# Optimization experiments

Measured on AMD Instinct MI355X. Metric: run time of the kernel, lower is better.

## Reference

```python
import jax, jax.numpy as jnp
import numpy as np

N = 524288   # tokens (accounts)
D = 9        # num_prop_size
E = 2        # expert_size
H = 128      # expert MLP hidden
M = 32       # moe_out
O = 2        # output_size
K = 1        # top-k
LOSS_COF = 0.01
EPS = 1e-10


def setup_inputs() -> dict:
    key = jax.random.key(0)
    ks = jax.random.split(key, 10)
    f32 = jnp.float32
    return {
        "num_prop": jax.random.normal(ks[0], (N, D), f32),
        "cat_prop": jax.random.normal(ks[1], (N, 3), f32),
        "w_gate": jax.random.normal(ks[2], (D, E), f32) * 0.1,
        "W1": jax.random.normal(ks[3], (E, D, H), f32) * 0.1,
        "b1": jax.random.normal(ks[4], (E, H), f32) * 0.01,
        "W2": jax.random.normal(ks[5], (E, H, M), f32) * 0.1,
        "b2": jax.random.normal(ks[6], (E, M), f32) * 0.01,
        "Wout": jax.random.normal(ks[7], (M, O), f32) * 0.1,
        "bout": jax.random.normal(ks[8], (O,), f32) * 0.01,
        "k": K,
    }


def _cv_squared(x):
    # torch: x.var() (unbiased) / (x.mean()**2 + eps)
    return jnp.var(x, ddof=1) / (jnp.mean(x) ** 2 + EPS)


def reference(num_prop, cat_prop, w_gate, W1, b1, W2, b2, Wout, bout, k):
    x = num_prop                                   # eval mode: dropout = identity
    n, e = x.shape[0], w_gate.shape[1]

    # --- top-k gating (eval: clean logits, no noise) ---
    logits = x @ w_gate                            # [N, E]
    top_logits, top_idx = jax.lax.top_k(logits, min(k + 1, e))
    top_k_gates = jax.nn.softmax(top_logits[:, :k], axis=1)   # [N, k]
    rows = jnp.arange(n)[:, None]
    gates = jnp.zeros_like(logits).at[rows, top_idx[:, :k]].set(top_k_gates)  # [N, E]

    importance = gates.sum(axis=0)                 # [E]
    load = (gates > 0).astype(jnp.float32).sum(axis=0)  # [E]
    loss = (_cv_squared(importance) + _cv_squared(load)) * LOSS_COF

    # --- experts: per-expert 2-layer MLP, computed dense (E=2) then gated combine ---
    h = jax.nn.relu(jnp.einsum("nd,edh->neh", x, W1) + b1)    # [N, E, H]
    y_e = jnp.einsum("neh,ehm->nem", h, W2) + b2              # [N, E, M]
    y = jnp.einsum("ne,nem->nm", gates, y_e)                  # [N, M]

    out = y @ Wout + bout                                     # [N, O]
    return (out, loss)
```

## Files before the change

kernel.cpp:

```cpp
#include <hip/hip_runtime.h>

#define NTOK 524288
#define TPB  256
#define NBLK (NTOK / TPB)

__device__ __forceinline__ float bf2f(unsigned short u) {
    union { unsigned int i; float f; } v;
    v.i = ((unsigned int)u) << 16;
    return v.f;
}

__device__ __forceinline__ float ldq(const void* p, int i, bool f32) {
    if (f32) return ((const float*)p)[i];
    return bf2f(((const unsigned short*)p)[i]);
}

__global__ void prep_kernel(const void* __restrict__ num_prop,
                            const void* __restrict__ wgate,
                            const void* __restrict__ W1,
                            const void* __restrict__ b1,
                            const void* __restrict__ W2,
                            const void* __restrict__ b2,
                            const void* __restrict__ Wout,
                            const void* __restrict__ bout,
                            unsigned int* __restrict__ cnt1,
                            int* __restrict__ flag,
                            float* __restrict__ bpp,
                            float* __restrict__ wgf,
                            float* __restrict__ wpack)
{
    __shared__ unsigned int bad;
    __shared__ int sflag;
    const int t = threadIdx.x;
    if (t == 0) { bad = 0u; *cnt1 = 0u; }
    __syncthreads();
    if (t < 72) {
        const unsigned short* u = (const unsigned short*)num_prop;
        int e = (u[t] >> 7) & 0xFF;
        if (e < 64 || e > 191) atomicOr(&bad, 1u);
    }
    __syncthreads();
    if (t == 0) { sflag = (int)bad; *flag = (int)bad; }
    __syncthreads();
    const bool f32 = (sflag != 0);

    if (t < 18) wgf[t] = ldq(wgate, t, f32);

    if (t < 4) {
        int e = t >> 1, o = t & 1;
        float acc = ldq(bout, o, f32);
        for (int m = 0; m < 32; ++m)
            acc += ldq(b2, e * 32 + m, f32) * ldq(Wout, m * 2 + o, f32);
        bpp[t] = acc;
    }

    const int e = t >> 7;
    const int j = t & 127;
    float p0 = 0.f, p1 = 0.f;
    for (int m = 0; m < 32; ++m) {
        float w = ldq(W2, (e * 128 + j) * 32 + m, f32);
        p0 += w * ldq(Wout, m * 2 + 0, f32);
        p1 += w * ldq(Wout, m * 2 + 1, f32);
    }
    float* dst = wpack + e * 1536 + j * 12;
    #pragma unroll
    for (int d = 0; d < 9; ++d)
        dst[d] = ldq(W1, (e * 9 + d) * 128 + j, f32);
    dst[9]  = ldq(b1, e * 128 + j, f32);
    dst[10] = p0;
    dst[11] = p1;
}

__global__ __launch_bounds__(TPB, 8)
void moe_main(const void* __restrict__ xg,
              const int* __restrict__ flag,
              const float* __restrict__ wgf,
              const float* __restrict__ bpp,
              const float* __restrict__ wpack,
              unsigned int* __restrict__ cnt1,
              float2* __restrict__ out)
{
    __shared__ __align__(16) float xs[TPB * 9];
    __shared__ unsigned char smap[TPB];
    __shared__ unsigned int wcnt[4];

    const int tid  = threadIdx.x;
    const int lane = tid & 63;
    const int wave = tid >> 6;

    const bool f32 = (*flag) != 0;
    const int gbase = blockIdx.x * (TPB * 9);
    if (f32) {
        const float* xf = (const float*)xg;
        #pragma unroll
        for (int i = 0; i < 9; ++i)
            xs[tid + i * TPB] = xf[gbase + tid + i * TPB];
    } else {
        const unsigned short* xu = (const unsigned short*)xg;
        for (int i = tid; i < TPB * 9; i += TPB)
            xs[i] = bf2f(xu[gbase + i]);
    }
    __syncthreads();

    float l0 = 0.f, l1 = 0.f;
    #pragma unroll
    for (int d = 0; d < 9; ++d) {
        float xv = xs[tid * 9 + d];
        l0 = fmaf(xv, wgf[d * 2 + 0], l0);
        l1 = fmaf(xv, wgf[d * 2 + 1], l1);
    }
    const bool e1 = l1 > l0;

    unsigned long long bal = __ballot(e1);
    if (lane == 0) wcnt[wave] = (unsigned int)__popcll(bal);
    __syncthreads();
    int pre = 0, tot = 0;
    #pragma unroll
    for (int w = 0; w < 4; ++w) {
        int c = (int)wcnt[w];
        if (w < wave) pre += c;
        tot += c;
    }
    const int n1 = tot;
    const int n0 = TPB - n1;
    const int p1 = pre + (int)__popcll(bal & ((1ull << lane) - 1ull));
    const int slot = e1 ? (n0 + p1) : (tid - p1);
    smap[slot] = (unsigned char)tid;
    if (tid == 0) atomicAdd(cnt1, (unsigned int)n1);
    __syncthreads();

    const int t = (int)smap[tid];
    float x[9];
    #pragma unroll
    for (int d = 0; d < 9; ++d) x[d] = xs[t * 9 + d];

    const int wbase = __builtin_amdgcn_readfirstlane(tid) & 192;
    const int n0u   = __builtin_amdgcn_readfirstlane(n0);

    float2 res;
    if (n0u <= wbase || n0u >= wbase + 64) {
        const int ew = (n0u <= wbase) ? 1 : 0;
        const float* wp = wpack + ew * 1536;
        float a0 = bpp[ew * 2 + 0], a1 = bpp[ew * 2 + 1];
        #pragma unroll 2
        for (int jp = 0; jp < 64; ++jp) {
            const float* r0 = wp + jp * 24;
            const float* r1 = r0 + 12;
            float h0 = r0[9], h1 = r1[9];
            #pragma unroll
            for (int d = 0; d < 9; ++d) {
                h0 = fmaf(x[d], r0[d], h0);
                h1 = fmaf(x[d], r1[d], h1);
            }
            h0 = fmaxf(h0, 0.f);
            h1 = fmaxf(h1, 0.f);
            a0 = fmaf(h0, r0[10], a0); a1 = fmaf(h0, r0[11], a1);
            a0 = fmaf(h1, r1[10], a0); a1 = fmaf(h1, r1[11], a1);
        }
        res.x = a0; res.y = a1;
    } else {
        const bool em = (tid >= n0u);
        float a00 = bpp[0], a01 = bpp[1], a10 = bpp[2], a11 = bpp[3];
        #pragma unroll 4
        for (int j = 0; j < 128; ++j) {
            const float* r0 = wpack + j * 12;
            const float* r1 = wpack + 1536 + j * 12;
            float h0 = r0[9], h1 = r1[9];
            #pragma unroll
            for (int d = 0; d < 9; ++d) {
                h0 = fmaf(x[d], r0[d], h0);
                h1 = fmaf(x[d], r1[d], h1);
            }
            h0 = fmaxf(h0, 0.f);
            h1 = fmaxf(h1, 0.f);
            a00 = fmaf(h0, r0[10], a00); a01 = fmaf(h0, r0[11], a01);
            a10 = fmaf(h1, r1[10], a10); a11 = fmaf(h1, r1[11], a11);
        }
        res.x = em ? a10 : a00;
        res.y = em ? a11 : a01;
    }

    __syncthreads();
    ((float2*)xs)[t] = res;
    __syncthreads();
    out[blockIdx.x * TPB + tid] = ((float2*)xs)[tid];
}

__global__ void finalize_kernel(const unsigned int* __restrict__ cnt1,
                                float* __restrict__ loss_out)
{
    double c1 = (double)(*cnt1);
    double c0 = (double)NTOK - c1;
    double diff = c0 - c1;
    double mean = (double)NTOK * 0.5;
    double var  = 0.5 * diff * diff;
    double cv2  = var / (mean * mean + 1e-10);
    *loss_out = (float)(0.02 * cv2);
}

extern "C" void kernel_launch(void* const* d_in, const int* in_sizes, int n_in,
                              void* d_out, int out_size, void* d_ws, size_t ws_size,
                              hipStream_t stream) {
    const void* num_prop = d_in[0];
    const void* w_gate   = d_in[2];
    const void* W1       = d_in[3];
    const void* b1       = d_in[4];
    const void* W2       = d_in[5];
    const void* b2       = d_in[6];
    const void* Wout     = d_in[7];
    const void* bout     = d_in[8];

    char* ws = (char*)d_ws;
    unsigned int* cnt1 = (unsigned int*)ws;
    int* flag          = (int*)(ws + 8);
    float* bpp         = (float*)(ws + 16);
    float* wgf         = (float*)(ws + 64);
    float* wpack       = (float*)(ws + 192);

    float*  outf = (float*)d_out;
    float2* out2 = (float2*)d_out;

    hipLaunchKernelGGL(prep_kernel, dim3(1), dim3(256), 0, stream,
                       num_prop, w_gate, W1, b1, W2, b2, Wout, bout,
                       cnt1, flag, bpp, wgf, wpack);
    hipLaunchKernelGGL(moe_main, dim3(NBLK), dim3(TPB), 0, stream,
                       num_prop, flag, wgf, bpp, wpack, cnt1, out2);
    hipLaunchKernelGGL(finalize_kernel, dim3(1), dim3(1), 0, stream,
                       cnt1, outf + (size_t)NTOK * 2);
}
```

Baseline: 149.6 us.

## Process four tokens per thread to amortize weight loads across tokens

Each block now handles 1024 tokens with 256 threads, so every thread computes four expert-sorted tokens and each weight row load is reused across four tokens. The packed weight rows are padded to 16 floats so they can be fetched with aligned vector loads, and launch bounds drop to 2 blocks per CU to allow more registers. In exchange, mixed-expert waves are more likely because each wave now spans 256 sorted slots, and those waves run the costlier both-experts path. There are also 4x fewer blocks and higher register pressure.

```diff
diff --git a/kernel.cpp b/kernel.cpp
--- a/kernel.cpp
+++ b/kernel.cpp
@@ -2,7 +2,8 @@
 
 #define NTOK 524288
 #define TPB  256
-#define NBLK (NTOK / TPB)
+#define TOKB 1024
+#define NBLK (NTOK / TOKB)
 
 __device__ __forceinline__ float bf2f(unsigned short u) {
     union { unsigned int i; float f; } v;
@@ -62,16 +63,17 @@
         p0 += w * ldq(Wout, m * 2 + 0, f32);
         p1 += w * ldq(Wout, m * 2 + 1, f32);
     }
-    float* dst = wpack + e * 1536 + j * 12;
+    float* dst = wpack + e * 2048 + j * 16;
     #pragma unroll
     for (int d = 0; d < 9; ++d)
         dst[d] = ldq(W1, (e * 9 + d) * 128 + j, f32);
     dst[9]  = ldq(b1, e * 128 + j, f32);
     dst[10] = p0;
     dst[11] = p1;
-}
-
-__global__ __launch_bounds__(TPB, 8)
+    dst[12] = 0.f; dst[13] = 0.f; dst[14] = 0.f; dst[15] = 0.f;
+}
+
+__global__ __launch_bounds__(TPB, 2)
 void moe_main(const void* __restrict__ xg,
               const int* __restrict__ flag,
               const float* __restrict__ wgf,
@@ -80,110 +82,154 @@
               unsigned int* __restrict__ cnt1,
               float2* __restrict__ out)
 {
-    __shared__ __align__(16) float xs[TPB * 9];
-    __shared__ unsigned char smap[TPB];
-    __shared__ unsigned int wcnt[4];
+    __shared__ __align__(16) float xs[TOKB * 9];
+    __shared__ unsigned short smap[TOKB];
+    __shared__ unsigned int wcnt[16];
 
     const int tid  = threadIdx.x;
     const int lane = tid & 63;
     const int wave = tid >> 6;
 
     const bool f32 = (*flag) != 0;
-    const int gbase = blockIdx.x * (TPB * 9);
+    const int gbase = blockIdx.x * (TOKB * 9);
     if (f32) {
         const float* xf = (const float*)xg;
         #pragma unroll
-        for (int i = 0; i < 9; ++i)
+        for (int i = 0; i < 36; ++i)
             xs[tid + i * TPB] = xf[gbase + tid + i * TPB];
     } else {
         const unsigned short* xu = (const unsigned short*)xg;
-        for (int i = tid; i < TPB * 9; i += TPB)
+        for (int i = tid; i < TOKB * 9; i += TPB)
             xs[i] = bf2f(xu[gbase + i]);
     }
     __syncthreads();
 
-    float l0 = 0.f, l1 = 0.f;
+    bool e1g[4];
+    unsigned long long balg[4];
+    #pragma unroll
+    for (int g = 0; g < 4; ++g) {
+        float l0 = 0.f, l1 = 0.f;
+        #pragma unroll
+        for (int d = 0; d < 9; ++d) {
+            float xv = xs[(g * 256 + tid) * 9 + d];
+            l0 = fmaf(xv, wgf[d * 2 + 0], l0);
+            l1 = fmaf(xv, wgf[d * 2 + 1], l1);
+        }
+        e1g[g] = l1 > l0;
+        balg[g] = __ballot(e1g[g]);
+        if (lane == 0) wcnt[g * 4 + wave] = (unsigned int)__popcll(balg[g]);
+    }
+    __syncthreads();
+
+    int pres[16]; int run = 0;
+    #pragma unroll
+    for (int c = 0; c < 16; ++c) { pres[c] = run; run += (int)wcnt[c]; }
+    const int n1 = run;
+    const int n0 = TOKB - n1;
+    const unsigned long long below = (1ull << lane) - 1ull;
+    #pragma unroll
+    for (int g = 0; g < 4; ++g) {
+        const int tok = g * 256 + tid;
+        const int pr  = pres[g * 4 + wave] + (int)__popcll(balg[g] & below);
+        const int slot = e1g[g] ? (n0 + pr) : (tok - pr);
+        smap[slot] = (unsigned short)tok;
+    }
+    if (tid == 0) atomicAdd(cnt1, (unsigned int)n1);
+    __syncthreads();
+
+    const int s0 = tid * 4;
+    const int tk0 = (int)smap[s0 + 0], tk1 = (int)smap[s0 + 1];
+    const int tk2 = (int)smap[s0 + 2], tk3 = (int)smap[s0 + 3];
+    float x0[9], x1[9], x2[9], x3[9];
     #pragma unroll
     for (int d = 0; d < 9; ++d) {
-        float xv = xs[tid * 9 + d];
-        l0 = fmaf(xv, wgf[d * 2 + 0], l0);
-        l1 = fmaf(xv, wgf[d * 2 + 1], l1);
-    }
-    const bool e1 = l1 > l0;
-
-    unsigned long long bal = __ballot(e1);
-    if (lane == 0) wcnt[wave] = (unsigned int)__popcll(bal);
-    __syncthreads();
-    int pre = 0, tot = 0;
-    #pragma unroll
-    for (int w = 0; w < 4; ++w) {
-        int c = (int)wcnt[w];
-        if (w < wave) pre += c;
-        tot += c;
-    }
-    const int n1 = tot;
-    const int n0 = TPB - n1;
-    const int p1 = pre + (int)__popcll(bal & ((1ull << lane) - 1ull));
-    const int slot = e1 ? (n0 + p1) : (tid - p1);
-    smap[slot] = (unsigned char)tid;
-    if (tid == 0) atomicAdd(cnt1, (unsigned int)n1);
-    __syncthreads();
-
-    const int t = (int)smap[tid];
-    float x[9];
-    #pragma unroll
-    for (int d = 0; d < 9; ++d) x[d] = xs[t * 9 + d];
-
-    const int wbase = __builtin_amdgcn_readfirstlane(tid) & 192;
+        x0[d] = xs[tk0 * 9 + d];
+        x1[d] = xs[tk1 * 9 + d];
+        x2[d] = xs[tk2 * 9 + d];
+        x3[d] = xs[tk3 * 9 + d];
+    }
+
+    const int wslot = __builtin_amdgcn_readfirstlane(wave) << 8;
     const int n0u   = __builtin_amdgcn_readfirstlane(n0);
 
-    float2 res;
-    if (n0u <= wbase || n0u >= wbase + 64) {
-        const int ew = (n0u <= wbase) ? 1 : 0;
-        const float* wp = wpack + ew * 1536;
-        float a0 = bpp[ew * 2 + 0], a1 = bpp[ew * 2 + 1];
+    float2 r0v, r1v, r2v, r3v;
+    if (n0u <= wslot || n0u >= wslot + 256) {
+        const int ew = (n0u <= wslot) ? 1 : 0;
+        const float* wp = wpack + ew * 2048;
+        const float b0 = bpp[ew * 2 + 0], b1v = bpp[ew * 2 + 1];
+        float a00 = b0, a01 = b1v, a10 = b0, a11 = b1v;
+        float a20 = b0, a21 = b1v, a30 = b0, a31 = b1v;
         #pragma unroll 2
-        for (int jp = 0; jp < 64; ++jp) {
-            const float* r0 = wp + jp * 24;
-            const float* r1 = r0 + 12;
-            float h0 = r0[9], h1 = r1[9];
+        for (int j = 0; j < 128; ++j) {
+            const float* r = wp + j * 16;
+            float h0 = r[9], h1 = r[9], h2 = r[9], h3 = r[9];
             #pragma unroll
             for (int d = 0; d < 9; ++d) {
-                h0 = fmaf(x[d], r0[d], h0);
-                h1 = fmaf(x[d], r1[d], h1);
+                const float w = r[d];
+                h0 = fmaf(x0[d], w, h0);
+                h1 = fmaf(x1[d], w, h1);
+                h2 = fmaf(x2[d], w, h2);
+                h3 = fmaf(x3[d], w, h3);
             }
-            h0 = fmaxf(h0, 0.f);
-            h1 = fmaxf(h1, 0.f);
-            a0 = fmaf(h0, r0[10], a0); a1 = fmaf(h0, r0[11], a1);
-            a0 = fmaf(h1, r1[10], a0); a1 = fmaf(h1, r1[11], a1);
+            h0 = fmaxf(h0, 0.f); h1 = fmaxf(h1, 0.f);
+            h2 = fmaxf(h2, 0.f); h3 = fmaxf(h3, 0.f);
+            const float wa = r[10], wb = r[11];
+            a00 = fmaf(h0, wa, a00); a01 = fmaf(h0, wb, a01);
+            a10 = fmaf(h1, wa, a10); a11 = fmaf(h1, wb, a11);
+            a20 = fmaf(h2, wa, a20); a21 = fmaf(h2, wb, a21);
+            a30 = fmaf(h3, wa, a30); a31 = fmaf(h3, wb, a31);
         }
-        res.x = a0; res.y = a1;
+        r0v.x = a00; r0v.y = a01; r1v.x = a10; r1v.y = a11;
+        r2v.x = a20; r2v.y = a21; r3v.x = a30; r3v.y = a31;
     } else {
-        const bool em = (tid >= n0u);
-        float a00 = bpp[0], a01 = bpp[1], a10 = bpp[2], a11 = bpp[3];
-        #pragma unroll 4
+        float A0[4], A1[4], A2[4], A3[4];
+        #pragma unroll
+        for (int k = 0; k < 4; ++k) { A0[k] = bpp[0]; A1[k] = bpp[1]; A2[k] = bpp[2]; A3[k] = bpp[3]; }
         for (int j = 0; j < 128; ++j) {
-            const float* r0 = wpack + j * 12;
-            const float* r1 = wpack + 1536 + j * 12;
-            float h0 = r0[9], h1 = r1[9];
+            const float* p0 = wpack + j * 16;
+            const float* p1 = wpack + 2048 + j * 16;
+            float h00 = p0[9], h01 = p1[9];
+            float h10 = p0[9], h11 = p1[9];
+            float h20 = p0[9], h21 = p1[9];
+            float h30 = p0[9], h31 = p1[9];
             #pragma unroll
             for (int d = 0; d < 9; ++d) {
-                h0 = fmaf(x[d], r0[d], h0);
-                h1 = fmaf(x[d], r1[d], h1);
+                const float w0 = p0[d], w1 = p1[d];
+                h00 = fmaf(x0[d], w0, h00); h01 = fmaf(x0[d], w1, h01);
+                h10 = fmaf(x1[d], w0, h10); h11 = fmaf(x1[d], w1, h11);
+                h20 = fmaf(x2[d], w0, h20); h21 = fmaf(x2[d], w1, h21);
+                h30 = fmaf(x3[d], w0, h30); h31 = fmaf(x3[d], w1, h31);
             }
-            h0 = fmaxf(h0, 0.f);
-            h1 = fmaxf(h1, 0.f);
-            a00 = fmaf(h0, r0[10], a00); a01 = fmaf(h0, r0[11], a01);
-            a10 = fmaf(h1, r1[10], a10); a11 = fmaf(h1, r1[11], a11);
+            h00 = fmaxf(h00, 0.f); h01 = fmaxf(h01, 0.f);
+            h10 = fmaxf(h10, 0.f); h11 = fmaxf(h11, 0.f);
+            h20 = fmaxf(h20, 0.f); h21 = fmaxf(h21, 0.f);
+            h30 = fmaxf(h30, 0.f); h31 = fmaxf(h31, 0.f);
+            const float wa0 = p0[10], wb0 = p0[11], wa1 = p1[10], wb1 = p1[11];
+            A0[0] = fmaf(h00, wa0, A0[0]); A1[0] = fmaf(h00, wb0, A1[0]);
+            A2[0] = fmaf(h01, wa1, A2[0]); A3[0] = fmaf(h01, wb1, A3[0]);
+            A0[1] = fmaf(h10, wa0, A0[1]); A1[1] = fmaf(h10, wb0, A1[1]);
+            A2[1] = fmaf(h11, wa1, A2[1]); A3[1] = fmaf(h11, wb1, A3[1]);
+            A0[2] = fmaf(h20, wa0, A0[2]); A1[2] = fmaf(h20, wb0, A1[2]);
+            A2[2] = fmaf(h21, wa1, A2[2]); A3[2] = fmaf(h21, wb1, A3[2]);
+            A0[3] = fmaf(h30, wa0, A0[3]); A1[3] = fmaf(h30, wb0, A1[3]);
+            A2[3] = fmaf(h31, wa1, A2[3]); A3[3] = fmaf(h31, wb1, A3[3]);
         }
-        res.x = em ? a10 : a00;
-        res.y = em ? a11 : a01;
-    }
-
-    __syncthreads();
-    ((float2*)xs)[t] = res;
-    __syncthreads();
-    out[blockIdx.x * TPB + tid] = ((float2*)xs)[tid];
+        const bool e0s = (s0 + 0) >= n0u, e1s = (s0 + 1) >= n0u;
+        const bool e2s = (s0 + 2) >= n0u, e3s = (s0 + 3) >= n0u;
+        r0v.x = e0s ? A2[0] : A0[0]; r0v.y = e0s ? A3[0] : A1[0];
+        r1v.x = e1s ? A2[1] : A0[1]; r1v.y = e1s ? A3[1] : A1[1];
+        r2v.x = e2s ? A2[2] : A0[2]; r2v.y = e2s ? A3[2] : A1[2];
+        r3v.x = e3s ? A2[3] : A0[3]; r3v.y = e3s ? A3[3] : A1[3];
+    }
+
+    __syncthreads();
+    float2* ob = (float2*)xs;
+    ob[tk0] = r0v; ob[tk1] = r1v; ob[tk2] = r2v; ob[tk3] = r3v;
+    __syncthreads();
+    const int obase = blockIdx.x * TOKB;
+    #pragma unroll
+    for (int g = 0; g < 4; ++g)
+        out[obase + g * 256 + tid] = ob[g * 256 + tid];
 }
 
 __global__ void finalize_kernel(const unsigned int* __restrict__ cnt1,
```

Result: slower. 153.4 us (+2.6%).

## Compute expert first layer with bf16x3-split MFMA instead of scalar FMAs

Applied to the files above, without the earlier changes.

Replaces the per-thread scalar FMA hidden-layer loop with MFMA 16x16x32 bf16 instructions. Inputs and W1 are split into hi/lo bf16 parts (hi*hi + lo*hi + hi*lo), and the bias is folded in through a constant-one column, so accuracy stays close to fp32. Both experts are computed for all tokens and the gated result is selected per token, which removes the token sort and the per-wave expert branching. It also vectorises the input load with float4 and moves the load count to per-wave atomics. The cost is extra prep packing, more registers from dropping the occupancy hint, and some residual precision loss from the split-bf16 scheme.

```diff
diff --git a/kernel.cpp b/kernel.cpp
--- a/kernel.cpp
+++ b/kernel.cpp
@@ -3,16 +3,26 @@
 #define NTOK 524288
 #define TPB  256
 #define NBLK (NTOK / TPB)
+
+typedef __attribute__((ext_vector_type(8))) short short8v;
+typedef __attribute__((ext_vector_type(4))) float float4v;
+
+union FragU { uint4 u; short8v s; };
 
 __device__ __forceinline__ float bf2f(unsigned short u) {
     union { unsigned int i; float f; } v;
     v.i = ((unsigned int)u) << 16;
     return v.f;
 }
-
 __device__ __forceinline__ float ldq(const void* p, int i, bool f32) {
     if (f32) return ((const float*)p)[i];
     return bf2f(((const unsigned short*)p)[i]);
+}
+__device__ __forceinline__ unsigned short btrunc(float w) {
+    return (unsigned short)(__float_as_uint(w) >> 16);
+}
+__device__ __forceinline__ float hif(float w) {
+    return __uint_as_float(__float_as_uint(w) & 0xFFFF0000u);
 }
 
 __global__ void prep_kernel(const void* __restrict__ num_prop,
@@ -25,9 +35,11 @@
                             const void* __restrict__ bout,
                             unsigned int* __restrict__ cnt1,
                             int* __restrict__ flag,
-                            float* __restrict__ bpp,
+                            float* __restrict__ bppf,
                             float* __restrict__ wgf,
-                            float* __restrict__ wpack)
+                            float* __restrict__ w2f,
+                            float* __restrict__ wpackF,
+                            unsigned int* __restrict__ wfragB)
 {
     __shared__ unsigned int bad;
     __shared__ int sflag;
@@ -51,52 +63,101 @@
         float acc = ldq(bout, o, f32);
         for (int m = 0; m < 32; ++m)
             acc += ldq(b2, e * 32 + m, f32) * ldq(Wout, m * 2 + o, f32);
-        bpp[t] = acc;
-    }
-
-    const int e = t >> 7;
-    const int j = t & 127;
-    float p0 = 0.f, p1 = 0.f;
-    for (int m = 0; m < 32; ++m) {
-        float w = ldq(W2, (e * 128 + j) * 32 + m, f32);
-        p0 += w * ldq(Wout, m * 2 + 0, f32);
-        p1 += w * ldq(Wout, m * 2 + 1, f32);
-    }
-    float* dst = wpack + e * 1536 + j * 12;
-    #pragma unroll
-    for (int d = 0; d < 9; ++d)
-        dst[d] = ldq(W1, (e * 9 + d) * 128 + j, f32);
-    dst[9]  = ldq(b1, e * 128 + j, f32);
-    dst[10] = p0;
-    dst[11] = p1;
-}
-
-__global__ __launch_bounds__(TPB, 8)
+        bppf[t] = acc;
+    }
+
+    {
+        const int e = t >> 7, j = t & 127;
+        float p0 = 0.f, p1 = 0.f;
+        for (int m = 0; m < 32; ++m) {
+            float w = ldq(W2, (e * 128 + j) * 32 + m, f32);
+            p0 += w * ldq(Wout, m * 2 + 0, f32);
+            p1 += w * ldq(Wout, m * 2 + 1, f32);
+        }
+        w2f[e * 256 + j * 2 + 0] = p0;
+        w2f[e * 256 + j * 2 + 1] = p1;
+        float* dst = wpackF + e * 1536 + j * 12;
+        #pragma unroll
+        for (int d = 0; d < 9; ++d)
+            dst[d] = ldq(W1, (e * 9 + d) * 128 + j, f32);
+        dst[9]  = ldq(b1, e * 128 + j, f32);
+        dst[10] = p0;
+        dst[11] = p1;
+    }
+
+    for (int q = 0; q < 4; ++q) {
+        const int idx = t + q * 256;
+        const int e  = idx >> 9;
+        const int t8 = (idx >> 6) & 7;
+        const int l  = idx & 63;
+        const int j  = t8 * 16 + (l & 15);
+        const int kg = l >> 4;
+        const float bb = ldq(b1, e * 128 + j, f32);
+        unsigned int u4[4];
+        #pragma unroll
+        for (int i = 0; i < 4; ++i) {
+            unsigned short v[2];
+            #pragma unroll
+            for (int h = 0; h < 2; ++h) {
+                const int s = kg * 8 + 2 * i + h;
+                unsigned short r = 0;
+                if (s <= 8) {
+                    float w = ldq(W1, (e * 9 + s) * 128 + j, f32);
+                    r = btrunc(w);
+                } else if (s <= 17) {
+                    float w = ldq(W1, (e * 9 + (s - 9)) * 128 + j, f32);
+                    r = btrunc(w);
+                } else if (s <= 26) {
+                    float w = ldq(W1, (e * 9 + (s - 18)) * 128 + j, f32);
+                    r = btrunc(w - hif(w));
+                } else if (s == 27) {
+                    r = btrunc(bb);
+                } else if (s == 28) {
+                    r = btrunc(bb - hif(bb));
+                }
+                v[h] = r;
+            }
+            u4[i] = (unsigned int)v[0] | ((unsigned int)v[1] << 16);
+        }
+        #pragma unroll
+        for (int i = 0; i < 4; ++i) wfragB[idx * 4 + i] = u4[i];
+    }
+}
+
+__global__ __launch_bounds__(TPB)
 void moe_main(const void* __restrict__ xg,
               const int* __restrict__ flag,
               const float* __restrict__ wgf,
-              const float* __restrict__ bpp,
-              const float* __restrict__ wpack,
+              const float* __restrict__ bppf,
+              const float* __restrict__ w2f,
+              const float* __restrict__ wpackF,
+              const unsigned int* __restrict__ wfragB,
               unsigned int* __restrict__ cnt1,
               float2* __restrict__ out)
 {
     __shared__ __align__(16) float xs[TPB * 9];
-    __shared__ unsigned char smap[TPB];
-    __shared__ unsigned int wcnt[4];
+    __shared__ __align__(16) unsigned int xpk[TPB * 20];
+    __shared__ float2 ob[TPB];
+    __shared__ unsigned char eflag[TPB];
 
     const int tid  = threadIdx.x;
     const int lane = tid & 63;
     const int wave = tid >> 6;
-
     const bool f32 = (*flag) != 0;
-    const int gbase = blockIdx.x * (TPB * 9);
+    const int tbase = blockIdx.x * TPB;
+
     if (f32) {
-        const float* xf = (const float*)xg;
-        #pragma unroll
-        for (int i = 0; i < 9; ++i)
-            xs[tid + i * TPB] = xf[gbase + tid + i * TPB];
+        const float4* xf4 = (const float4*)xg;
+        float4* xsv = (float4*)xs;
+        const int g4 = blockIdx.x * (TPB * 9 / 4);
+        #pragma unroll
+        for (int i = 0; i < 3; ++i) {
+            const int idx = i * 256 + tid;
+            if (idx < TPB * 9 / 4) xsv[idx] = xf4[g4 + idx];
+        }
     } else {
         const unsigned short* xu = (const unsigned short*)xg;
+        const int gbase = blockIdx.x * (TPB * 9);
         for (int i = tid; i < TPB * 9; i += TPB)
             xs[i] = bf2f(xu[gbase + i]);
     }
@@ -105,85 +166,137 @@
     float l0 = 0.f, l1 = 0.f;
     #pragma unroll
     for (int d = 0; d < 9; ++d) {
-        float xv = xs[tid * 9 + d];
+        const float xv = xs[tid * 9 + d];
         l0 = fmaf(xv, wgf[d * 2 + 0], l0);
         l1 = fmaf(xv, wgf[d * 2 + 1], l1);
     }
     const bool e1 = l1 > l0;
-
+    eflag[tid] = e1 ? 1 : 0;
     unsigned long long bal = __ballot(e1);
-    if (lane == 0) wcnt[wave] = (unsigned int)__popcll(bal);
-    __syncthreads();
-    int pre = 0, tot = 0;
-    #pragma unroll
-    for (int w = 0; w < 4; ++w) {
-        int c = (int)wcnt[w];
-        if (w < wave) pre += c;
-        tot += c;
-    }
-    const int n1 = tot;
-    const int n0 = TPB - n1;
-    const int p1 = pre + (int)__popcll(bal & ((1ull << lane) - 1ull));
-    const int slot = e1 ? (n0 + p1) : (tid - p1);
-    smap[slot] = (unsigned char)tid;
-    if (tid == 0) atomicAdd(cnt1, (unsigned int)n1);
-    __syncthreads();
-
-    const int t = (int)smap[tid];
-    float x[9];
-    #pragma unroll
-    for (int d = 0; d < 9; ++d) x[d] = xs[t * 9 + d];
-
-    const int wbase = __builtin_amdgcn_readfirstlane(tid) & 192;
-    const int n0u   = __builtin_amdgcn_readfirstlane(n0);
-
-    float2 res;
-    if (n0u <= wbase || n0u >= wbase + 64) {
-        const int ew = (n0u <= wbase) ? 1 : 0;
-        const float* wp = wpack + ew * 1536;
-        float a0 = bpp[ew * 2 + 0], a1 = bpp[ew * 2 + 1];
-        #pragma unroll 2
-        for (int jp = 0; jp < 64; ++jp) {
-            const float* r0 = wp + jp * 24;
-            const float* r1 = r0 + 12;
+    if (lane == 0) atomicAdd(cnt1, (unsigned int)__popcll(bal));
+
+    if (!f32) {
+        float xr[9];
+        #pragma unroll
+        for (int d = 0; d < 9; ++d) xr[d] = xs[tid * 9 + d];
+        float a00 = bppf[0], a01 = bppf[1], a10 = bppf[2], a11 = bppf[3];
+        for (int j = 0; j < 128; ++j) {
+            const float* r0 = wpackF + j * 12;
+            const float* r1 = wpackF + 1536 + j * 12;
             float h0 = r0[9], h1 = r1[9];
             #pragma unroll
             for (int d = 0; d < 9; ++d) {
-                h0 = fmaf(x[d], r0[d], h0);
-                h1 = fmaf(x[d], r1[d], h1);
-            }
-            h0 = fmaxf(h0, 0.f);
-            h1 = fmaxf(h1, 0.f);
-            a0 = fmaf(h0, r0[10], a0); a1 = fmaf(h0, r0[11], a1);
-            a0 = fmaf(h1, r1[10], a0); a1 = fmaf(h1, r1[11], a1);
-        }
-        res.x = a0; res.y = a1;
-    } else {
-        const bool em = (tid >= n0u);
-        float a00 = bpp[0], a01 = bpp[1], a10 = bpp[2], a11 = bpp[3];
-        #pragma unroll 4
-        for (int j = 0; j < 128; ++j) {
-            const float* r0 = wpack + j * 12;
-            const float* r1 = wpack + 1536 + j * 12;
-            float h0 = r0[9], h1 = r1[9];
-            #pragma unroll
-            for (int d = 0; d < 9; ++d) {
-                h0 = fmaf(x[d], r0[d], h0);
-                h1 = fmaf(x[d], r1[d], h1);
-            }
-            h0 = fmaxf(h0, 0.f);
-            h1 = fmaxf(h1, 0.f);
+                h0 = fmaf(xr[d], r0[d], h0);
+                h1 = fmaf(xr[d], r1[d], h1);
+            }
+            h0 = fmaxf(h0, 0.f); h1 = fmaxf(h1, 0.f);
             a00 = fmaf(h0, r0[10], a00); a01 = fmaf(h0, r0[11], a01);
             a10 = fmaf(h1, r1[10], a10); a11 = fmaf(h1, r1[11], a11);
         }
-        res.x = em ? a10 : a00;
-        res.y = em ? a11 : a01;
-    }
-
-    __syncthreads();
-    ((float2*)xs)[t] = res;
-    __syncthreads();
-    out[blockIdx.x * TPB + tid] = ((float2*)xs)[tid];
+        out[tbase + tid] = make_float2(e1 ? a10 : a00, e1 ? a11 : a01);
+        return;
+    }
+
+    {
+        unsigned short hv[9], lv[9];
+        #pragma unroll
+        for (int d = 0; d < 9; ++d) {
+            const float xv = xs[tid * 9 + d];
+            hv[d] = btrunc(xv);
+            lv[d] = btrunc(xv - hif(xv));
+        }
+        const unsigned int ONE = 0x3F80u;
+        #define PK(a,b) ((unsigned int)(a) | ((unsigned int)(b) << 16))
+        uint4* xp = (uint4*)&xpk[tid * 20];
+        xp[0] = make_uint4(PK(hv[0],hv[1]), PK(hv[2],hv[3]),
+                           PK(hv[4],hv[5]), PK(hv[6],hv[7]));
+        xp[1] = make_uint4(PK(hv[8],lv[0]), PK(lv[1],lv[2]),
+                           PK(lv[3],lv[4]), PK(lv[5],lv[6]));
+        xp[2] = make_uint4(PK(lv[7],lv[8]), PK(hv[0],hv[1]),
+                           PK(hv[2],hv[3]), PK(hv[4],hv[5]));
+        xp[3] = make_uint4(PK(hv[6],hv[7]), PK(hv[8],ONE),
+                           PK(ONE,0u), 0u);
+        #undef PK
+    }
+    __syncthreads();
+
+    FragU bw[16];
+    #pragma unroll
+    for (int et = 0; et < 16; ++et)
+        bw[et].u = ((const uint4*)wfragB)[et * 64 + lane];
+    float2 w2v[16];
+    #pragma unroll
+    for (int et = 0; et < 16; ++et) {
+        const int e = et >> 3, t8 = et & 7;
+        w2v[et] = ((const float2*)w2f)[e * 128 + t8 * 16 + (lane & 15)];
+    }
+    const float bp0 = bppf[0], bp1 = bppf[1], bp2 = bppf[2], bp3 = bppf[3];
+    const float4v zero4 = {0.f, 0.f, 0.f, 0.f};
+
+    #pragma unroll
+    for (int r = 0; r < 4; ++r) {
+        const int tb16 = wave * 64 + r * 16;
+        FragU av;
+        av.u = *(const uint4*)&xpk[(tb16 + (lane & 15)) * 20 + ((lane >> 4) << 2)];
+        const unsigned int efw =
+            *(const unsigned int*)&eflag[tb16 + ((lane >> 4) << 2)];
+
+        float4v d0[8], d1[8];
+        #pragma unroll
+        for (int t8 = 0; t8 < 8; ++t8)
+            d0[t8] = __builtin_amdgcn_mfma_f32_16x16x32_bf16(av.s, bw[t8].s, zero4, 0, 0, 0);
+        #pragma unroll
+        for (int t8 = 0; t8 < 8; ++t8)
+            d1[t8] = __builtin_amdgcn_mfma_f32_16x16x32_bf16(av.s, bw[8 + t8].s, zero4, 0, 0, 0);
+
+        float yx0 = 0.f, yx1 = 0.f, yx2 = 0.f, yx3 = 0.f;
+        float yy0 = 0.f, yy1 = 0.f, yy2 = 0.f, yy3 = 0.f;
+        const bool b0 = (efw >> 0)  & 1;
+        const bool b1b = (efw >> 8)  & 1;
+        const bool b2b = (efw >> 16) & 1;
+        const bool b3b = (efw >> 24) & 1;
+        #pragma unroll
+        for (int t8 = 0; t8 < 8; ++t8) {
+            const float4v v0 = d0[t8], v1 = d1[t8];
+            const float2 wa = w2v[t8], wb = w2v[8 + t8];
+            {
+                float h = b0 ? fmaxf(v1[0], 0.f) : fmaxf(v0[0], 0.f);
+                yx0 = fmaf(h, b0 ? wb.x : wa.x, yx0);
+                yy0 = fmaf(h, b0 ? wb.y : wa.y, yy0);
+            }
+            {
+                float h = b1b ? fmaxf(v1[1], 0.f) : fmaxf(v0[1], 0.f);
+                yx1 = fmaf(h, b1b ? wb.x : wa.x, yx1);
+                yy1 = fmaf(h, b1b ? wb.y : wa.y, yy1);
+            }
+            {
+                float h = b2b ? fmaxf(v1[2], 0.f) : fmaxf(v0[2], 0.f);
+                yx2 = fmaf(h, b2b ? wb.x : wa.x, yx2);
+                yy2 = fmaf(h, b2b ? wb.y : wa.y, yy2);
+            }
+            {
+                float h = b3b ? fmaxf(v1[3], 0.f) : fmaxf(v0[3], 0.f);
+                yx3 = fmaf(h, b3b ? wb.x : wa.x, yx3);
+                yy3 = fmaf(h, b3b ? wb.y : wa.y, yy3);
+            }
+        }
+        #pragma unroll
+        for (int m = 1; m < 16; m <<= 1) {
+            yx0 += __shfl_xor(yx0, m, 16); yy0 += __shfl_xor(yy0, m, 16);
+            yx1 += __shfl_xor(yx1, m, 16); yy1 += __shfl_xor(yy1, m, 16);
+            yx2 += __shfl_xor(yx2, m, 16); yy2 += __shfl_xor(yy2, m, 16);
+            yx3 += __shfl_xor(yx3, m, 16); yy3 += __shfl_xor(yy3, m, 16);
+        }
+        if ((lane & 15) == 0) {
+            const int tk = tb16 + ((lane >> 4) << 2);
+            ob[tk + 0] = make_float2(yx0 + (b0  ? bp2 : bp0), yy0 + (b0  ? bp3 : bp1));
+            ob[tk + 1] = make_float2(yx1 + (b1b ? bp2 : bp0), yy1 + (b1b ? bp3 : bp1));
+            ob[tk + 2] = make_float2(yx2 + (b2b ? bp2 : bp0), yy2 + (b2b ? bp3 : bp1));
+            ob[tk + 3] = make_float2(yx3 + (b3b ? bp2 : bp0), yy3 + (b3b ? bp3 : bp1));
+        }
+    }
+    __syncthreads();
+    out[tbase + tid] = ob[tid];
 }
 
 __global__ void finalize_kernel(const unsigned int* __restrict__ cnt1,
@@ -211,20 +324,23 @@
     const void* bout     = d_in[8];
 
     char* ws = (char*)d_ws;
-    unsigned int* cnt1 = (unsigned int*)ws;
-    int* flag          = (int*)(ws + 8);
-    float* bpp         = (float*)(ws + 16);
-    float* wgf         = (float*)(ws + 64);
-    float* wpack       = (float*)(ws + 192);
+    unsigned int* cnt1   = (unsigned int*)ws;
+    int* flag            = (int*)(ws + 8);
+    float* bppf          = (float*)(ws + 16);
+    float* wgf           = (float*)(ws + 64);
+    float* w2f           = (float*)(ws + 192);
+    float* wpackF        = (float*)(ws + 2304);
+    unsigned int* wfragB = (unsigned int*)(ws + 14592);
 
     float*  outf = (float*)d_out;
     float2* out2 = (float2*)d_out;
 
     hipLaunchKernelGGL(prep_kernel, dim3(1), dim3(256), 0, stream,
                        num_prop, w_gate, W1, b1, W2, b2, Wout, bout,
-                       cnt1, flag, bpp, wgf, wpack);
+                       cnt1, flag, bppf, wgf, w2f, wpackF, wfragB);
     hipLaunchKernelGGL(moe_main, dim3(NBLK), dim3(TPB), 0, stream,
-                       num_prop, flag, wgf, bpp, wpack, cnt1, out2);
+                       num_prop, flag, wgf, bppf, w2f, wpackF, wfragB,
+                       cnt1, out2);
     hipLaunchKernelGGL(finalize_kernel, dim3(1), dim3(1), 0, stream,
                        cnt1, outf + (size_t)NTOK * 2);
 }
```

New measurement: 206.5 us. 1.38x slower.
